# Optimization experiments

Hardware: AMD Instinct MI355X
Metric: run time of the kernel (lower is better)

The kernel has to match this reference:

```python
import jax, jax.numpy as jnp
import numpy as np

B, SEQ, S, DIM_IN, DIM_K, DIM_V = 4, 2048, 128, 512, 64, 64
L = SEQ + 2 * S
NEG = -1e30  # stand-in for log(0) in the tril mask (finite for stable vjp)


def _layernorm(x, g, b, eps=1e-5):
    m = jnp.mean(x, axis=-1, keepdims=True)
    v = jnp.var(x, axis=-1, keepdims=True)
    return (x - m) / jnp.sqrt(v + eps) * g + b


def setup_inputs() -> dict:
    key = jax.random.key(0)
    ks = jax.random.split(key, 18)
    w = lambda k, shape, s=0.02: (jax.random.normal(k, shape, jnp.float32) * s)
    inp = {
        "x": jax.random.normal(ks[0], (B, L, DIM_IN), jnp.float32),
        "Wq": w(ks[1], (DIM_IN, DIM_K)),
        "Wk": w(ks[2], (DIM_IN, DIM_K)),
        "Wv": w(ks[3], (DIM_IN, DIM_V)),
        "Wq_s": w(ks[4], (DIM_IN, DIM_K)),
        "Wk_s": w(ks[5], (DIM_IN, DIM_K)),
        "Wv_s": w(ks[6], (DIM_IN, DIM_V)),
        "Wq_e": w(ks[7], (DIM_IN, DIM_K)),
        "Wk_e": w(ks[8], (DIM_IN, DIM_K)),
        "Wv_e": w(ks[9], (DIM_IN, DIM_V)),
        "ln_g": jnp.ones((DIM_IN,), jnp.float32),
        "ln_b": jnp.zeros((DIM_IN,), jnp.float32),
        "ln_s_g": jnp.ones((DIM_IN,), jnp.float32),
        "ln_s_b": jnp.zeros((DIM_IN,), jnp.float32),
        "ln_e_g": jnp.ones((DIM_IN,), jnp.float32),
        "ln_e_b": jnp.zeros((DIM_IN,), jnp.float32),
        "cope_emb": jax.random.normal(ks[10], (DIM_K, S), jnp.float32),
        "offset": 0,
    }
    return inp


def reference(x, Wq, Wk, Wv, Wq_s, Wk_s, Wv_s, Wq_e, Wk_e, Wv_e,
              ln_g, ln_b, ln_s_g, ln_s_b, ln_e_g, ln_e_b, cope_emb, offset):
    # extract_state: first/last state_len tokens
    xs, xm, xe = x[:, :S], x[:, S:L - S], x[:, -S:]
    xm = _layernorm(xm, ln_g, ln_b)
    xs = _layernorm(xs, ln_s_g, ln_s_b)
    xe = _layernorm(xe, ln_e_g, ln_e_b)

    q, k, v = xm @ Wq, xm @ Wk, xm @ Wv          # (B, SEQ, dk/dv)
    q_s, k_s, v_s = xs @ Wq_s, xs @ Wk_s, xs @ Wv_s
    q_e, k_e, v_e = xe @ Wq_e, xe @ Wk_e, xe @ Wv_e

    # CoPE bias over the non-state block
    logits = jnp.einsum('bqd,bkd->bqk', q, k)    # (B, SEQ, SEQ)
    gates = jax.nn.sigmoid(logits)
    pos = jnp.flip(jnp.cumsum(jnp.flip(gates, -1), axis=-1), -1)
    pos = jnp.minimum(pos, jnp.float32(S - 1))
    pos_ceil = jnp.ceil(pos).astype(jnp.int32)
    pos_floor = jnp.floor(pos).astype(jnp.int32)
    logits_int = jnp.einsum('bqd,dk->bqk', q, cope_emb)  # (B, SEQ, S)
    logits_c = jnp.take_along_axis(logits_int, pos_ceil, axis=-1)
    logits_f = jnp.take_along_axis(logits_int, pos_floor, axis=-1)
    wfrac = pos - pos_floor.astype(pos.dtype)
    bias = logits_c * wfrac + logits_f * (1.0 - wfrac)   # (B, SEQ, SEQ)

    q_full = jnp.concatenate([q_s, q, q_e], axis=1)      # (B, L, dk)
    k_full = jnp.concatenate([k_s, k, k_e], axis=1)
    v_full = jnp.concatenate([v_s, v, v_e], axis=1)

    # explicit tril log-mask bias with CoPE injected in the middle block
    tri = jnp.tril(jnp.ones((L, L), dtype=bool))
    attn_bias = jnp.where(tri, 0.0, NEG).astype(jnp.float32)
    attn_bias = jnp.broadcast_to(attn_bias, (B, L, L))
    attn_bias = attn_bias.at[:, S:L - S, S:L - S].add(bias)

    scale = 1.0 / jnp.sqrt(jnp.float32(DIM_K))
    scores = jnp.einsum('bqd,bkd->bqk', q_full, k_full) * scale + attn_bias
    att = jax.nn.softmax(scores, axis=-1)
    return jnp.einsum('bqk,bkd->bqd', att, v_full)       # (B, L, dv)
```

## Files before the change

kernel.cpp:

```cpp
#include <hip/hip_runtime.h>
#include <math.h>

#define B_    4
#define SEQ_  2048
#define S_    128
#define L_    2304
#define DIN   512
#define DK    64
#define NEGINF (-1e30f)
#define SCALE 0.125f
#define NCOLS 2176
#define NMID  8192
#define NEDGE 1024
#define LE    2304

typedef _Float16 f16;
typedef __attribute__((ext_vector_type(8))) _Float16 half8;
typedef __attribute__((ext_vector_type(4))) float f32x4;

union U4 { uint4 u; f16 h[8]; };

__global__ __launch_bounds__(256) void k_wsplit(
    const float* __restrict__ Wq,  const float* __restrict__ Wk,  const float* __restrict__ Wv,
    const float* __restrict__ Wqs, const float* __restrict__ Wks, const float* __restrict__ Wvs,
    const float* __restrict__ Wqe, const float* __restrict__ Wke, const float* __restrict__ Wve,
    f16* __restrict__ Wsp)
{
    __shared__ float xs[64 * 68];
    const int kt  = blockIdx.x;
    const int mat = blockIdx.y;
    const float* W;
    switch (mat) {
        case 0: W = Wq;  break; case 1: W = Wk;  break; case 2: W = Wv;  break;
        case 3: W = Wqs; break; case 4: W = Wks; break; case 5: W = Wvs; break;
        case 6: W = Wqe; break; case 7: W = Wke; break; default: W = Wve; break;
    }
    const int tid = threadIdx.x;
    const int k0  = kt * 64;
    #pragma unroll
    for (int i = 0; i < 4; ++i) {
        int g = tid + 256 * i;
        int k = g >> 4, c4 = g & 15;
        *(float4*)(xs + k * 68 + c4 * 4) = ((const float4*)W)[(size_t)(k0 + k) * 16 + c4];
    }
    __syncthreads();
    const int col = tid & 63, hf = tid >> 6;
    const int kk0 = hf * 16;
    U4 hi0, hi1, lo0, lo1;
    #pragma unroll
    for (int j = 0; j < 8; ++j) {
        float v0 = xs[(kk0 + j) * 68 + col];
        float v1 = xs[(kk0 + 8 + j) * 68 + col];
        hi0.h[j] = (f16)v0; lo0.h[j] = (f16)(v0 - (float)hi0.h[j]);
        hi1.h[j] = (f16)v1; lo1.h[j] = (f16)(v1 - (float)hi1.h[j]);
    }
    f16* dst = Wsp + (size_t)mat * 65536 + (size_t)col * 1024 + k0 + kk0;
    *(uint4*)(dst)       = hi0.u;
    *(uint4*)(dst + 8)   = hi1.u;
    *(uint4*)(dst + 512) = lo0.u;
    *(uint4*)(dst + 520) = lo1.u;
}

__global__ __launch_bounds__(256) void k_proj(
    const float* __restrict__ x, const f16* __restrict__ Wsp,
    const float* __restrict__ g0, const float* __restrict__ b0,
    const float* __restrict__ gs, const float* __restrict__ bs,
    const float* __restrict__ ge, const float* __restrict__ be,
    f16* __restrict__ qsp, f16* __restrict__ ksp, f16* __restrict__ vhT)
{
    __shared__ f16 As[64 * 136];
    __shared__ f16 Bs[64 * 136];
    __shared__ float mean_s[64], rstd_s[64];
    const int tid  = threadIdx.x;
    const int row0 = blockIdx.x * 64;
    const int rseq = row0 % L_;
    const int seg  = (rseq < S_) ? 0 : (rseq >= L_ - S_) ? 2 : 1;
    const int m    = blockIdx.y;
    const int mat  = m + ((seg == 0) ? 3 : (seg == 2) ? 6 : 0);
    const f16* Wc  = Wsp + (size_t)mat * 65536;
    const float* gg = (seg == 0) ? gs : (seg == 2) ? ge : g0;
    const float* bb = (seg == 0) ? bs : (seg == 2) ? be : b0;

    {
        const int rr = tid >> 2, qq = tid & 3;
        const float4* xr = (const float4*)(x + (size_t)(row0 + rr) * DIN) + qq * 32;
        float s = 0.f, s2 = 0.f;
        #pragma unroll
        for (int i = 0; i < 32; ++i) {
            float4 v = xr[i];
            s  += v.x + v.y + v.z + v.w;
            s2 += v.x * v.x + v.y * v.y + v.z * v.z + v.w * v.w;
        }
        s  += __shfl_xor(s, 1);  s  += __shfl_xor(s, 2);
        s2 += __shfl_xor(s2, 1); s2 += __shfl_xor(s2, 2);
        if (qq == 0) {
            float mean = s * (1.f / DIN);
            mean_s[rr] = mean;
            rstd_s[rr] = rsqrtf(s2 * (1.f / DIN) - mean * mean + 1e-5f);
        }
    }

    const int w = tid >> 6, lane = tid & 63;
    const int cl = lane & 15, quad = lane >> 4;
    const int r0 = 32 * (w >> 1), c0 = 32 * (w & 1);

    f32x4 acc[2][2];
    #pragma unroll
    for (int i = 0; i < 2; ++i)
        #pragma unroll
        for (int j = 0; j < 2; ++j) acc[i][j] = 0.f;

    for (int kc = 0; kc < DIN; kc += 64) {
        __syncthreads();
        #pragma unroll
        for (int i = 0; i < 2; ++i) {
            int g = tid + 256 * i;
            int r = g >> 3, c8 = g & 7;
            const float* xp = x + (size_t)(row0 + r) * DIN + kc + c8 * 8;
            float4 a0 = *(const float4*)xp;
            float4 a1 = *(const float4*)(xp + 4);
            float4 gA = *(const float4*)(gg + kc + c8 * 8);
            float4 gB = *(const float4*)(gg + kc + c8 * 8 + 4);
            float4 bA = *(const float4*)(bb + kc + c8 * 8);
            float4 bB = *(const float4*)(bb + kc + c8 * 8 + 4);
            float mean = mean_s[r], rstd = rstd_s[r];
            float n[8];
            n[0] = (a0.x - mean) * rstd * gA.x + bA.x;
            n[1] = (a0.y - mean) * rstd * gA.y + bA.y;
            n[2] = (a0.z - mean) * rstd * gA.z + bA.z;
            n[3] = (a0.w - mean) * rstd * gA.w + bA.w;
            n[4] = (a1.x - mean) * rstd * gB.x + bB.x;
            n[5] = (a1.y - mean) * rstd * gB.y + bB.y;
            n[6] = (a1.z - mean) * rstd * gB.z + bB.z;
            n[7] = (a1.w - mean) * rstd * gB.w + bB.w;
            U4 hi, lo;
            #pragma unroll
            for (int j = 0; j < 8; ++j) {
                hi.h[j] = (f16)n[j];
                lo.h[j] = (f16)(n[j] - (float)hi.h[j]);
            }
            *(uint4*)(As + r * 136 + c8 * 8)      = hi.u;
            *(uint4*)(As + r * 136 + 64 + c8 * 8) = lo.u;
        }
        #pragma unroll
        for (int i = 0; i < 2; ++i) {
            int g = tid + 256 * i;
            int col = g >> 3, c8 = g & 7;
            const f16* src = Wc + (size_t)col * 1024 + kc + c8 * 8;
            *(uint4*)(Bs + col * 136 + c8 * 8)      = *(const uint4*)(src);
            *(uint4*)(Bs + col * 136 + 64 + c8 * 8) = *(const uint4*)(src + 512);
        }
        __syncthreads();
        #pragma unroll
        for (int h = 0; h < 2; ++h) {
            half8 ah[2], al[2], bh[2], bl[2];
            #pragma unroll
            for (int rs = 0; rs < 2; ++rs) {
                const f16* base = As + (r0 + 16 * rs + cl) * 136 + h * 32 + quad * 8;
                ah[rs] = *(const half8*)(base);
                al[rs] = *(const half8*)(base + 64);
            }
            #pragma unroll
            for (int cs = 0; cs < 2; ++cs) {
                const f16* base = Bs + (c0 + 16 * cs + cl) * 136 + h * 32 + quad * 8;
                bh[cs] = *(const half8*)(base);
                bl[cs] = *(const half8*)(base + 64);
            }
            #pragma unroll
            for (int rs = 0; rs < 2; ++rs)
                #pragma unroll
                for (int cs = 0; cs < 2; ++cs) {
                    acc[rs][cs] = __builtin_amdgcn_mfma_f32_16x16x32_f16(ah[rs], bh[cs], acc[rs][cs], 0, 0, 0);
                    acc[rs][cs] = __builtin_amdgcn_mfma_f32_16x16x32_f16(ah[rs], bl[cs], acc[rs][cs], 0, 0, 0);
                    acc[rs][cs] = __builtin_amdgcn_mfma_f32_16x16x32_f16(al[rs], bh[cs], acc[rs][cs], 0, 0, 0);
                }
        }
    }

    const int bI = row0 / L_;
    const int rb = row0 - bI * L_;
    f16* sp = (m == 0) ? qsp : ksp;
    #pragma unroll
    for (int rs = 0; rs < 2; ++rs)
        #pragma unroll
        for (int cs = 0; cs < 2; ++cs)
            #pragma unroll
            for (int r = 0; r < 4; ++r) {
                int lrow = r0 + 16 * rs + quad * 4 + r;
                int col  = c0 + 16 * cs + cl;
                float v  = acc[rs][cs][r];
                size_t grow = (size_t)(row0 + lrow);
                if (m < 2) {
                    f16 hv = (f16)v;
                    sp[grow * 128 + col]      = hv;
                    sp[grow * 128 + 64 + col] = (f16)(v - (float)hv);
                } else {
                    vhT[(size_t)(bI * 64 + col) * L_ + rb + lrow] = (f16)v;
                }
            }
}

__global__ __launch_bounds__(256) void k_dots(
    const f16* __restrict__ qsp, const f16* __restrict__ ksp,
    float* __restrict__ D32, float* __restrict__ G, float* __restrict__ De32)
{
    const int bx = blockIdx.x, by = blockIdx.y;
    const bool edge = (bx >= 64);
    int b, q0 = 0;
    size_t qrow0;
    if (!edge) {
        if (by >= 17) return;
        b = bx >> 4;
        q0 = (bx * 128) & 2047;
        qrow0 = (size_t)b * L_ + S_ + q0;
    } else {
        int ex = bx - 64;
        b = ex >> 1;
        int half = ex & 1;
        if (half == 0 && by > 0) return;
        qrow0 = (size_t)b * L_ + (half ? 2176 : 0);
    }
    const int col0 = by * 128;
    const size_t krow0 = (size_t)b * L_ + col0;

    __shared__ f16 Qs[128 * 136];
    __shared__ f16 Ks[128 * 136];
    const int tid = threadIdx.x;

    #pragma unroll
    for (int i = 0; i < 8; ++i) {
        int g = tid + 256 * i;
        int r = g >> 4, c = g & 15;
        *(uint4*)(Qs + r * 136 + c * 8) = *(const uint4*)(qsp + (qrow0 + r) * 128 + c * 8);
        *(uint4*)(Ks + r * 136 + c * 8) = *(const uint4*)(ksp + (krow0 + r) * 128 + c * 8);
    }
    __syncthreads();

    const int w = tid >> 6, lane = tid & 63;
    const int cl = lane & 15, quad = lane >> 4;

    f32x4 acc[2][8];
    #pragma unroll
    for (int i = 0; i < 2; ++i)
        #pragma unroll
        for (int j = 0; j < 8; ++j) acc[i][j] = 0.f;

    #pragma unroll
    for (int h = 0; h < 2; ++h) {
        half8 ah[2], al[2];
        #pragma unroll
        for (int rs = 0; rs < 2; ++rs) {
            const f16* base = Qs + (32 * w + 16 * rs + cl) * 136 + h * 32 + quad * 8;
            ah[rs] = *(const half8*)(base);
            al[rs] = *(const half8*)(base + 64);
        }
        #pragma unroll
        for (int cq = 0; cq < 2; ++cq) {
            half8 bh[4], bl[4];
            #pragma unroll
            for (int cc = 0; cc < 4; ++cc) {
                const f16* base = Ks + (16 * (cq * 4 + cc) + cl) * 136 + h * 32 + quad * 8;
                bh[cc] = *(const half8*)(base);
                bl[cc] = *(const half8*)(base + 64);
            }
            #pragma unroll
            for (int rs = 0; rs < 2; ++rs)
                #pragma unroll
                for (int cc = 0; cc < 4; ++cc) {
                    int c = cq * 4 + cc;
                    acc[rs][c] = __builtin_amdgcn_mfma_f32_16x16x32_f16(ah[rs], bh[cc], acc[rs][c], 0, 0, 0);
                    acc[rs][c] = __builtin_amdgcn_mfma_f32_16x16x32_f16(ah[rs], bl[cc], acc[rs][c], 0, 0, 0);
                    acc[rs][c] = __builtin_amdgcn_mfma_f32_16x16x32_f16(al[rs], bh[cc], acc[rs][c], 0, 0, 0);
                }
        }
    }

    if (!edge) {
        const int gr0 = bx * 128;
        const bool writeD = (by == 0) || ((by - 1) <= (q0 >> 7));
        if (writeD) {
            #pragma unroll
            for (int rs = 0; rs < 2; ++rs)
                #pragma unroll
                for (int c = 0; c < 8; ++c)
                    #pragma unroll
                    for (int r = 0; r < 4; ++r) {
                        int mrow = gr0 + 32 * w + 16 * rs + quad * 4 + r;
                        int n    = col0 + 16 * c + cl;
                        D32[(size_t)mrow * NCOLS + n] = acc[rs][c][r];
                    }
        }
        if (by >= 1) {
            const int chm = 2 * (by - 1);
            #pragma unroll
            for (int rs = 0; rs < 2; ++rs)
                #pragma unroll
                for (int r = 0; r < 4; ++r) {
                    float sA = 0.f, sB = 0.f;
                    #pragma unroll
                    for (int cc = 0; cc < 4; ++cc) {
                        sA += 1.f / (1.f + __expf(-acc[rs][cc][r]));
                        sB += 1.f / (1.f + __expf(-acc[rs][4 + cc][r]));
                    }
                    #pragma unroll
                    for (int off = 1; off < 16; off <<= 1) {
                        sA += __shfl_xor(sA, off);
                        sB += __shfl_xor(sB, off);
                    }
                    if (cl == 0) {
                        int row = gr0 + 32 * w + 16 * rs + quad * 4 + r;
                        G[(size_t)row * 32 + chm]     = sA;
                        G[(size_t)row * 32 + chm + 1] = sB;
                    }
                }
        }
    } else {
        const int er0 = (bx - 64) * 128;
        #pragma unroll
        for (int rs = 0; rs < 2; ++rs)
            #pragma unroll
            for (int c = 0; c < 8; ++c)
                #pragma unroll
                for (int r = 0; r < 4; ++r) {
                    int erow = er0 + 32 * w + 16 * rs + quad * 4 + r;
                    int n    = col0 + 16 * c + cl;
                    De32[(size_t)erow * LE + n] = acc[rs][c][r];
                }
    }
}

__global__ __launch_bounds__(256) void k_scan(
    const f16* __restrict__ qsp, const float* __restrict__ cope,
    const float* __restrict__ G,
    const float* __restrict__ D32, f16* __restrict__ Dp,
    const float* __restrict__ De32, f16* __restrict__ Dep)
{
    __shared__ f16   qvh[128];
    __shared__ float li[128];
    __shared__ float Gs[32];
    __shared__ float Gsf[32];
    __shared__ float wmax[4], wsum[4];
    const int tid = threadIdx.x;
    const int gr  = blockIdx.x;
    const int lane = tid & 63, wid = tid >> 6;

    if (gr < NMID) {
        const int b = gr >> 11;
        const int q = gr & 2047;
        const size_t grow = (size_t)b * L_ + S_ + q;
        const int qlim = (q & ~63) + 64;

        if (tid < 16) ((uint4*)qvh)[tid] = ((const uint4*)(qsp + grow * 128))[tid];
        if (tid >= 16 && tid < 24)
            ((float4*)Gs)[tid - 16] = ((const float4*)G)[(size_t)gr * 8 + tid - 16];
        __syncthreads();
        if (tid < 128) {
            float a = 0.f;
            #pragma unroll
            for (int d = 0; d < DK; ++d)
                a += ((float)qvh[d] + (float)qvh[64 + d]) * cope[d * S_ + tid];
            li[tid] = a;
        }
        if (tid >= 128 && tid < 160) {
            int c = tid - 128;
            float s = 0.f;
            for (int cc = c + 1; cc < 32; ++cc) s += Gs[cc];
            Gsf[c] = s;
        }

        const float* Sr = D32 + (size_t)gr * NCOLS;
        f16* Dr = Dp + (size_t)gr * NCOLS;
        const int j0 = tid * 8;
        const int cg = tid >> 3, sl = tid & 7;
        float dot[8], gte[8];
        float csum = 0.f;
        if (j0 < qlim) {
            float4 t0 = *(const float4*)(Sr + 128 + j0);
            float4 t1 = *(const float4*)(Sr + 128 + j0 + 4);
            dot[0] = t0.x; dot[1] = t0.y; dot[2] = t0.z; dot[3] = t0.w;
            dot[4] = t1.x; dot[5] = t1.y; dot[6] = t1.z; dot[7] = t1.w;
            #pragma unroll
            for (int jj = 0; jj < 8; ++jj) {
                gte[jj] = 1.f / (1.f + __expf(-dot[jj]));
                csum += gte[jj];
            }
        } else {
            #pragma unroll
            for (int jj = 0; jj < 8; ++jj) { dot[jj] = 0.f; gte[jj] = 0.f; }
        }
        float sv = (tid < 128) ? Sr[tid] * SCALE : NEGINF;

        float inc = csum;
        #pragma unroll
        for (int off = 1; off < 8; off <<= 1) {
            float u = __shfl_down(inc, off, 8);
            if (sl + off < 8) inc += u;
        }
        __syncthreads();
        float run = (inc - csum) + Gsf[cg];

        float p8[8];
        #pragma unroll
        for (int jj = 7; jj >= 0; --jj) {
            run += gte[jj];
            float pos = fminf(run, (float)(S_ - 1));
            float pfl = floorf(pos);
            int ic  = (int)ceilf(pos);
            int ifl = (int)pfl;
            float w = pos - pfl;
            float bias = li[ic] * w + li[ifl] * (1.f - w);
            p8[jj] = (j0 + jj <= q) ? dot[jj] * SCALE + bias : NEGINF;
        }

        float mx = sv;
        #pragma unroll
        for (int jj = 0; jj < 8; ++jj) mx = fmaxf(mx, p8[jj]);
        #pragma unroll
        for (int off = 1; off < 64; off <<= 1) mx = fmaxf(mx, __shfl_xor(mx, off));
        if (lane == 0) wmax[wid] = mx;
        __syncthreads();
        mx = fmaxf(fmaxf(wmax[0], wmax[1]), fmaxf(wmax[2], wmax[3]));

        float lsum = 0.f;
        float e8[8];
        #pragma unroll
        for (int jj = 0; jj < 8; ++jj) {
            e8[jj] = __expf(p8[jj] - mx);
            lsum += e8[jj];
        }
        float es = 0.f;
        if (tid < 128) { es = __expf(sv - mx); lsum += es; }
        #pragma unroll
        for (int off = 1; off < 64; off <<= 1) lsum += __shfl_xor(lsum, off);
        if (lane == 0) wsum[wid] = lsum;
        __syncthreads();
        float inv = 1.f / (wsum[0] + wsum[1] + wsum[2] + wsum[3]);

        if (j0 < qlim) {
            U4 o;
            #pragma unroll
            for (int jj = 0; jj < 8; ++jj) o.h[jj] = (f16)(e8[jj] * inv);
            *(uint4*)(Dr + 128 + j0) = o.u;
        }
        if (tid < 128) Dr[tid] = (f16)(es * inv);
    } else {
        const int er = gr - NMID;
        const int r  = er & 255;
        const int Q  = (r < 128) ? r : (2048 + r);
        const float* Er32 = De32 + (size_t)er * LE;
        f16* Er = Dep + (size_t)er * LE;

        float v[9];
        #pragma unroll
        for (int i = 0; i < 9; ++i) {
            int j = tid + 256 * i;
            float d = Er32[j];
            v[i] = (j <= Q) ? d * SCALE : NEGINF;
        }
        float mx = v[0];
        #pragma unroll
        for (int i = 1; i < 9; ++i) mx = fmaxf(mx, v[i]);
        #pragma unroll
        for (int off = 1; off < 64; off <<= 1) mx = fmaxf(mx, __shfl_xor(mx, off));
        if (lane == 0) wmax[wid] = mx;
        __syncthreads();
        mx = fmaxf(fmaxf(wmax[0], wmax[1]), fmaxf(wmax[2], wmax[3]));

        float lsum = 0.f;
        #pragma unroll
        for (int i = 0; i < 9; ++i) {
            v[i] = __expf(v[i] - mx);
            lsum += v[i];
        }
        #pragma unroll
        for (int off = 1; off < 64; off <<= 1) lsum += __shfl_xor(lsum, off);
        if (lane == 0) wsum[wid] = lsum;
        __syncthreads();
        float inv = 1.f / (wsum[0] + wsum[1] + wsum[2] + wsum[3]);

        #pragma unroll
        for (int i = 0; i < 9; ++i)
            Er[tid + 256 * i] = (f16)(v[i] * inv);
    }
}

__global__ __launch_bounds__(256) void k_pv(
    const f16* __restrict__ Pmid, const f16* __restrict__ Pedge,
    const f16* __restrict__ vhT,
    float* __restrict__ Opart, float* __restrict__ Oe)
{
    __shared__ f16 Ps[64 * 72];
    __shared__ f16 Vt[64 * 72];
    const int tid = threadIdx.x;
    const int bx  = blockIdx.x;
    const int ks  = blockIdx.y;
    const bool edge = (bx >= 128);

    const f16* Pb;
    size_t pitch;
    int row0, b, cap, cmax;
    float* outp;
    if (!edge) {
        row0 = bx * 64;
        b = row0 >> 11;
        int q0 = row0 & 2047;
        Pb = Pmid; pitch = NCOLS; cap = 34;
        cmax = (191 + q0) >> 6;
        outp = Opart + (size_t)ks * NMID * DK;
    } else {
        row0 = (bx - 128) * 64;
        b = row0 >> 8;
        int r0 = row0 & 255;
        Pb = Pedge; pitch = LE; cap = 36;
        int Qmax = (r0 < 128) ? (r0 + 63) : (2048 + r0 + 63);
        cmax = Qmax >> 6;
        outp = Oe + (size_t)ks * NEDGE * DK;
    }
    const int c_beg = ks * 9;
    int c_end = c_beg + 9;
    if (c_end > cap) c_end = cap;
    if (c_end > cmax + 1) c_end = cmax + 1;

    const int w = tid >> 6, lane = tid & 63;
    const int cl = lane & 15, quad = lane >> 4;
    f32x4 acc[4];
    #pragma unroll
    for (int c = 0; c < 4; ++c) acc[c] = 0.f;

    for (int ch = c_beg; ch < c_end; ++ch) {
        __syncthreads();
        #pragma unroll
        for (int i = 0; i < 2; ++i) {
            int g = tid + 256 * i;
            int r = g >> 3, c = g & 7;
            *(uint4*)(Ps + r * 72 + c * 8) =
                *(const uint4*)(Pb + (size_t)(row0 + r) * pitch + ch * 64 + c * 8);
            *(uint4*)(Vt + r * 72 + c * 8) =
                *(const uint4*)(vhT + (size_t)(b * 64 + r) * L_ + ch * 64 + c * 8);
        }
        __syncthreads();
        #pragma unroll
        for (int h = 0; h < 2; ++h) {
            half8 a = *(const half8*)(Ps + (16 * w + cl) * 72 + h * 32 + quad * 8);
            #pragma unroll
            for (int c = 0; c < 4; ++c) {
                half8 bv = *(const half8*)(Vt + (16 * c + cl) * 72 + h * 32 + quad * 8);
                acc[c] = __builtin_amdgcn_mfma_f32_16x16x32_f16(a, bv, acc[c], 0, 0, 0);
            }
        }
    }
    #pragma unroll
    for (int c = 0; c < 4; ++c)
        #pragma unroll
        for (int r = 0; r < 4; ++r) {
            int mrow = row0 + 16 * w + quad * 4 + r;
            int n    = 16 * c + cl;
            outp[(size_t)mrow * DK + n] = acc[c][r];
        }
}

__global__ __launch_bounds__(256) void k_merge(
    const float* __restrict__ Opart, const float* __restrict__ Oe,
    float* __restrict__ out)
{
    const int e = blockIdx.x * 256 + threadIdx.x;
    if (e < NMID * DK) {
        const int gr = e >> 6, c = e & 63;
        const int b  = gr >> 11, q = gr & 2047;
        const int NP = NMID * DK;
        float s = Opart[e] + Opart[e + NP] + Opart[e + 2 * NP] + Opart[e + 3 * NP];
        out[((size_t)b * L_ + S_ + q) * DK + c] = s;
    } else {
        const int e2 = e - NMID * DK;
        const int er = e2 >> 6, c = e2 & 63;
        const int b  = er >> 8, r = er & 255;
        const int gQ = (r < 128) ? r : (2048 + r);
        const int NP = NEDGE * DK;
        float s = Oe[e2] + Oe[e2 + NP] + Oe[e2 + 2 * NP] + Oe[e2 + 3 * NP];
        out[((size_t)b * L_ + gQ) * DK + c] = s;
    }
}

extern "C" void kernel_launch(void* const* d_in, const int* in_sizes, int n_in,
                              void* d_out, int out_size, void* d_ws, size_t ws_size,
                              hipStream_t stream)
{
    const float* x    = (const float*)d_in[0];
    const float* Wq   = (const float*)d_in[1];
    const float* Wk   = (const float*)d_in[2];
    const float* Wv   = (const float*)d_in[3];
    const float* Wqs  = (const float*)d_in[4];
    const float* Wks  = (const float*)d_in[5];
    const float* Wvs  = (const float*)d_in[6];
    const float* Wqe  = (const float*)d_in[7];
    const float* Wke  = (const float*)d_in[8];
    const float* Wve  = (const float*)d_in[9];
    const float* g0   = (const float*)d_in[10];
    const float* b0   = (const float*)d_in[11];
    const float* gs   = (const float*)d_in[12];
    const float* bs   = (const float*)d_in[13];
    const float* ge   = (const float*)d_in[14];
    const float* be   = (const float*)d_in[15];
    const float* cope = (const float*)d_in[16];

    const size_t NR = (size_t)B_ * L_;
    f16*   qsp   = (f16*)d_ws;
    f16*   ksp   = qsp + NR * 128;
    f16*   vhT   = ksp + NR * 128;
    f16*   Wsp   = vhT + NR * 64;
    float* G     = (float*)(Wsp + (size_t)9 * 65536);
    float* Opart = G + (size_t)NMID * 32;
    float* Oe    = Opart + (size_t)4 * NMID * DK;
    float* Dm32  = Oe + (size_t)4 * NEDGE * DK;
    float* De32  = Dm32 + (size_t)NMID * NCOLS;
    f16*   Dp    = (f16*)(De32 + (size_t)NEDGE * LE);
    f16*   Dep   = Dp + (size_t)NMID * NCOLS;
    float* out   = (float*)d_out;

    k_wsplit<<<dim3(8, 9), 256, 0, stream>>>(Wq, Wk, Wv, Wqs, Wks, Wvs,
                                             Wqe, Wke, Wve, Wsp);
    k_proj<<<dim3(144, 3), 256, 0, stream>>>(x, Wsp, g0, b0, gs, bs, ge, be,
                                             qsp, ksp, vhT);
    k_dots<<<dim3(72, 18), 256, 0, stream>>>(qsp, ksp, Dm32, G, De32);
    k_scan<<<NMID + NEDGE, 256, 0, stream>>>(qsp, cope, G, Dm32, Dp, De32, Dep);
    k_pv  <<<dim3(144, 4), 256, 0, stream>>>(Dp, Dep, vhT, Opart, Oe);
    k_merge<<<(NMID + NEDGE) * DK / 256, 256, 0, stream>>>(Opart, Oe, out);
}
```

Before: 195.4 us.

## Fuse Q/K/V projections into one block per 32-row tile

The projection kernel now computes all three outputs (Q, K, V) in a single block over a 32-row tile, instead of launching a separate block per matrix over 64-row tiles. The LayerNorm statistics and the normalized, hi/lo-split activations are computed once per tile rather than three times, and x is read once instead of three times. In exchange, each block stages all three weight slices in shared memory, which raises LDS use, and the grid shrinks from 432 to 288 blocks.

After: 194.6 us. About the same (-0.4%).

```diff
diff --git a/kernel.cpp b/kernel.cpp
--- a/kernel.cpp
+++ b/kernel.cpp
@@ -68,31 +68,29 @@
     const float* __restrict__ ge, const float* __restrict__ be,
     f16* __restrict__ qsp, f16* __restrict__ ksp, f16* __restrict__ vhT)
 {
-    __shared__ f16 As[64 * 136];
-    __shared__ f16 Bs[64 * 136];
-    __shared__ float mean_s[64], rstd_s[64];
+    __shared__ f16 As[32 * 136];
+    __shared__ f16 Bs[3 * 64 * 136];
+    __shared__ float mean_s[32], rstd_s[32];
     const int tid  = threadIdx.x;
-    const int row0 = blockIdx.x * 64;
+    const int row0 = blockIdx.x * 32;
     const int rseq = row0 % L_;
     const int seg  = (rseq < S_) ? 0 : (rseq >= L_ - S_) ? 2 : 1;
-    const int m    = blockIdx.y;
-    const int mat  = m + ((seg == 0) ? 3 : (seg == 2) ? 6 : 0);
-    const f16* Wc  = Wsp + (size_t)mat * 65536;
+    const int mat0 = (seg == 0) ? 3 : (seg == 2) ? 6 : 0;
     const float* gg = (seg == 0) ? gs : (seg == 2) ? ge : g0;
     const float* bb = (seg == 0) ? bs : (seg == 2) ? be : b0;
 
     {
-        const int rr = tid >> 2, qq = tid & 3;
-        const float4* xr = (const float4*)(x + (size_t)(row0 + rr) * DIN) + qq * 32;
+        const int rr = tid >> 3, qq = tid & 7;
+        const float4* xr = (const float4*)(x + (size_t)(row0 + rr) * DIN) + qq * 16;
         float s = 0.f, s2 = 0.f;
         #pragma unroll
-        for (int i = 0; i < 32; ++i) {
+        for (int i = 0; i < 16; ++i) {
             float4 v = xr[i];
             s  += v.x + v.y + v.z + v.w;
             s2 += v.x * v.x + v.y * v.y + v.z * v.z + v.w * v.w;
         }
-        s  += __shfl_xor(s, 1);  s  += __shfl_xor(s, 2);
-        s2 += __shfl_xor(s2, 1); s2 += __shfl_xor(s2, 2);
+        s  += __shfl_xor(s, 1);  s  += __shfl_xor(s, 2);  s  += __shfl_xor(s, 4);
+        s2 += __shfl_xor(s2, 1); s2 += __shfl_xor(s2, 2); s2 += __shfl_xor(s2, 4);
         if (qq == 0) {
             float mean = s * (1.f / DIN);
             mean_s[rr] = mean;
@@ -102,20 +100,18 @@
 
     const int w = tid >> 6, lane = tid & 63;
     const int cl = lane & 15, quad = lane >> 4;
-    const int r0 = 32 * (w >> 1), c0 = 32 * (w & 1);
-
-    f32x4 acc[2][2];
-    #pragma unroll
-    for (int i = 0; i < 2; ++i)
-        #pragma unroll
-        for (int j = 0; j < 2; ++j) acc[i][j] = 0.f;
+    const int r0 = 16 * (w >> 1), c0 = 32 * (w & 1);
+
+    f32x4 acc[3][2];
+    #pragma unroll
+    for (int m = 0; m < 3; ++m)
+        #pragma unroll
+        for (int j = 0; j < 2; ++j) acc[m][j] = 0.f;
 
     for (int kc = 0; kc < DIN; kc += 64) {
         __syncthreads();
-        #pragma unroll
-        for (int i = 0; i < 2; ++i) {
-            int g = tid + 256 * i;
-            int r = g >> 3, c8 = g & 7;
+        {
+            int r = tid >> 3, c8 = tid & 7;
             const float* xp = x + (size_t)(row0 + r) * DIN + kc + c8 * 8;
             float4 a0 = *(const float4*)xp;
             float4 a1 = *(const float4*)(xp + 4);
@@ -143,52 +139,50 @@
             *(uint4*)(As + r * 136 + 64 + c8 * 8) = lo.u;
         }
         #pragma unroll
-        for (int i = 0; i < 2; ++i) {
+        for (int i = 0; i < 6; ++i) {
             int g = tid + 256 * i;
-            int col = g >> 3, c8 = g & 7;
-            const f16* src = Wc + (size_t)col * 1024 + kc + c8 * 8;
-            *(uint4*)(Bs + col * 136 + c8 * 8)      = *(const uint4*)(src);
-            *(uint4*)(Bs + col * 136 + 64 + c8 * 8) = *(const uint4*)(src + 512);
+            int mm = g >> 9, rem = g & 511;
+            int col = rem >> 3, c8 = rem & 7;
+            const f16* src = Wsp + (size_t)(mat0 + mm) * 65536 + (size_t)col * 1024 + kc + c8 * 8;
+            f16* dst = Bs + mm * 8704 + col * 136 + c8 * 8;
+            *(uint4*)(dst)      = *(const uint4*)(src);
+            *(uint4*)(dst + 64) = *(const uint4*)(src + 512);
         }
         __syncthreads();
         #pragma unroll
         for (int h = 0; h < 2; ++h) {
-            half8 ah[2], al[2], bh[2], bl[2];
-            #pragma unroll
-            for (int rs = 0; rs < 2; ++rs) {
-                const f16* base = As + (r0 + 16 * rs + cl) * 136 + h * 32 + quad * 8;
-                ah[rs] = *(const half8*)(base);
-                al[rs] = *(const half8*)(base + 64);
+            half8 ah, al;
+            {
+                const f16* base = As + (r0 + cl) * 136 + h * 32 + quad * 8;
+                ah = *(const half8*)(base);
+                al = *(const half8*)(base + 64);
             }
             #pragma unroll
-            for (int cs = 0; cs < 2; ++cs) {
-                const f16* base = Bs + (c0 + 16 * cs + cl) * 136 + h * 32 + quad * 8;
-                bh[cs] = *(const half8*)(base);
-                bl[cs] = *(const half8*)(base + 64);
-            }
-            #pragma unroll
-            for (int rs = 0; rs < 2; ++rs)
+            for (int m = 0; m < 3; ++m)
                 #pragma unroll
                 for (int cs = 0; cs < 2; ++cs) {
-                    acc[rs][cs] = __builtin_amdgcn_mfma_f32_16x16x32_f16(ah[rs], bh[cs], acc[rs][cs], 0, 0, 0);
-                    acc[rs][cs] = __builtin_amdgcn_mfma_f32_16x16x32_f16(ah[rs], bl[cs], acc[rs][cs], 0, 0, 0);
-                    acc[rs][cs] = __builtin_amdgcn_mfma_f32_16x16x32_f16(al[rs], bh[cs], acc[rs][cs], 0, 0, 0);
+                    const f16* base = Bs + m * 8704 + (c0 + 16 * cs + cl) * 136 + h * 32 + quad * 8;
+                    half8 bh = *(const half8*)(base);
+                    half8 bl = *(const half8*)(base + 64);
+                    acc[m][cs] = __builtin_amdgcn_mfma_f32_16x16x32_f16(ah, bh, acc[m][cs], 0, 0, 0);
+                    acc[m][cs] = __builtin_amdgcn_mfma_f32_16x16x32_f16(ah, bl, acc[m][cs], 0, 0, 0);
+                    acc[m][cs] = __builtin_amdgcn_mfma_f32_16x16x32_f16(al, bh, acc[m][cs], 0, 0, 0);
                 }
         }
     }
 
     const int bI = row0 / L_;
     const int rb = row0 - bI * L_;
-    f16* sp = (m == 0) ? qsp : ksp;
-    #pragma unroll
-    for (int rs = 0; rs < 2; ++rs)
+    #pragma unroll
+    for (int m = 0; m < 3; ++m) {
+        f16* sp = (m == 0) ? qsp : ksp;
         #pragma unroll
         for (int cs = 0; cs < 2; ++cs)
             #pragma unroll
             for (int r = 0; r < 4; ++r) {
-                int lrow = r0 + 16 * rs + quad * 4 + r;
+                int lrow = r0 + quad * 4 + r;
                 int col  = c0 + 16 * cs + cl;
-                float v  = acc[rs][cs][r];
+                float v  = acc[m][cs][r];
                 size_t grow = (size_t)(row0 + lrow);
                 if (m < 2) {
                     f16 hv = (f16)v;
@@ -198,6 +192,7 @@
                     vhT[(size_t)(bI * 64 + col) * L_ + rb + lrow] = (f16)v;
                 }
             }
+    }
 }
 
 __global__ __launch_bounds__(256) void k_dots(
@@ -619,8 +614,8 @@
 
     k_wsplit<<<dim3(8, 9), 256, 0, stream>>>(Wq, Wk, Wv, Wqs, Wks, Wvs,
                                              Wqe, Wke, Wve, Wsp);
-    k_proj<<<dim3(144, 3), 256, 0, stream>>>(x, Wsp, g0, b0, gs, bs, ge, be,
-                                             qsp, ksp, vhT);
+    k_proj<<<288, 256, 0, stream>>>(x, Wsp, g0, b0, gs, bs, ge, be,
+                                    qsp, ksp, vhT);
     k_dots<<<dim3(72, 18), 256, 0, stream>>>(qsp, ksp, Dm32, G, De32);
     k_scan<<<NMID + NEDGE, 256, 0, stream>>>(qsp, cope, G, Dm32, Dp, De32, Dep);
     k_pv  <<<dim3(144, 4), 256, 0, stream>>>(Dp, Dep, vhT, Opart, Oe);
```
